# Optimization experiments

Hardware: AMD Instinct MI355X
Metric: run time of the kernel (lower is better)

The kernel has to match this reference:

```python
import jax, jax.numpy as jnp
import numpy as np

B, L, H, V = 16, 512, 256, 32000
HALF = H // 2
EPS_LN = 1e-5
EPS_NORM = 1e-12


def setup_inputs() -> dict:
    key = jax.random.key(0)
    ks = jax.random.split(key, 9)
    s = 0.02
    return {
        "seq": jax.random.randint(ks[0], (B, L), 0, V),
        "embed": jax.random.normal(ks[1], (V, H), jnp.float32) * s,
        "W1": jax.random.normal(ks[2], (2 * H, H), jnp.float32) * s,
        "b1": jnp.zeros((2 * H,), jnp.float32),
        "W2": jax.random.normal(ks[3], (H, 2 * H), jnp.float32) * s,
        "b2": jnp.zeros((H,), jnp.float32),
        "gamma": jnp.ones((H,), jnp.float32),
        "beta": jnp.zeros((H,), jnp.float32),
        "W_sem": jax.random.normal(ks[4], (HALF, H), jnp.float32) * s,
        "W_epi": jax.random.normal(ks[5], (HALF, H), jnp.float32) * s,
        "W_rp": jax.random.normal(ks[6], (H, H), jnp.float32) * s,
        "b_rp": jnp.zeros((H,), jnp.float32),
        "W_out": jax.random.normal(ks[7], (V, H), jnp.float32) * s,
        "b_out": jnp.zeros((V,), jnp.float32),
    }


def _l2norm(x):
    # F.normalize(dim=-1): x / max(||x||, eps)
    n = jnp.sqrt(jnp.sum(x * x, axis=-1, keepdims=True))
    return x / jnp.maximum(n, EPS_NORM)


def reference(seq, embed, W1, b1, W2, b2, gamma, beta, W_sem, W_epi, W_rp, b_rp, W_out, b_out):
    h = embed[seq]                                   # [B, L, H]
    ff = jnp.maximum(h @ W1.T + b1, 0.0) @ W2.T + b2  # MLP with 2H hidden
    x = h + ff
    mu = jnp.mean(x, axis=-1, keepdims=True)
    var = jnp.var(x, axis=-1, keepdims=True)
    h = (x - mu) / jnp.sqrt(var + EPS_LN) * gamma + beta  # LayerNorm

    ks_all = jnp.einsum('blh,kh->blk', h, W_sem)     # [B, L, HALF]
    ke_all = jnp.einsum('blh,kh->blk', h, W_epi)

    def step(carry, kv):
        M_s, M_e = carry
        k_s, k_e = kv                                 # [B, HALF] each
        kns = _l2norm(k_s)
        kne = _l2norm(k_e)
        vps = jnp.einsum('bij,bj->bi', M_s, kns)      # read from fast weights
        vpe = jnp.einsum('bij,bj->bi', M_e, kne)
        M_s = M_s + jnp.einsum('bi,bj->bij', k_s - vps, kns)  # delta-rule write
        M_e = M_e + jnp.einsum('bi,bj->bij', k_e - vpe, kne)
        return (M_s, M_e), None

    M0 = jnp.zeros((B, HALF, HALF), h.dtype)
    # scan over timesteps 0..L-2 (time-major)
    (M_s, M_e), _ = jax.lax.scan(
        step, (M0, M0),
        (jnp.swapaxes(ks_all[:, :-1], 0, 1), jnp.swapaxes(ke_all[:, :-1], 0, 1)))

    cs = jnp.einsum('bij,bj->bi', M_s, ks_all[:, -1])  # read with last-token query
    ce = jnp.einsum('bij,bj->bi', M_e, ke_all[:, -1])
    c = jnp.concatenate([cs, ce], axis=-1)             # [B, H]
    r = c @ W_rp.T + b_rp
    return r @ W_out.T + b_out                          # [B, V]
```

## Files before the change

kernel.cpp:

```cpp
#include <hip/hip_runtime.h>

#define B_ 16
#define L_ 512
#define H_ 256
#define V_ 32000
#define HALF_ 128

typedef __attribute__((ext_vector_type(8))) short short8;
typedef __attribute__((ext_vector_type(4))) float floatx4;

__device__ __forceinline__ unsigned short f2bf(float x) {
  unsigned int u = __float_as_uint(x);
  unsigned int r = (u + 0x7FFFu + ((u >> 16) & 1u)) >> 16;
  return (unsigned short)r;
}

__global__ void gather_kernel(const int* __restrict__ seq, const float* __restrict__ embed,
                              float* __restrict__ h, unsigned short* __restrict__ hbf) {
  int token = blockIdx.x;
  int lane = threadIdx.x;
  int row = seq[token];
  float4 v = ((const float4*)(embed + (size_t)row * H_))[lane];
  ((float4*)(h + (size_t)token * H_))[lane] = v;
  ushort4 b;
  b.x = f2bf(v.x); b.y = f2bf(v.y); b.z = f2bf(v.z); b.w = f2bf(v.w);
  *(ushort4*)(hbf + (size_t)token * H_ + lane * 4) = b;
}

__global__ void wconv_kernel(const float* __restrict__ W1, const float* __restrict__ W2,
                             const float* __restrict__ Ws, const float* __restrict__ We,
                             unsigned short* __restrict__ W1b, unsigned short* __restrict__ W2b,
                             unsigned short* __restrict__ Wcb) {
  int i = blockIdx.x * 256 + threadIdx.x;
  if (i < 131072) W1b[i] = f2bf(W1[i]);
  else if (i < 262144) W2b[i - 131072] = f2bf(W2[i - 131072]);
  else if (i < 294912) Wcb[i - 262144] = f2bf(Ws[i - 262144]);
  else Wcb[i - 262144] = f2bf(We[i - 294912]);
}

template <bool RELU, bool BIAS, bool RES, bool OUT_BF16>
__global__ __launch_bounds__(256) void gemm_mfma(const unsigned short* __restrict__ A,
                                                 const unsigned short* __restrict__ Bw,
                                                 const float* __restrict__ bias,
                                                 const float* __restrict__ Res,
                                                 float* __restrict__ Cf,
                                                 unsigned short* __restrict__ Cb,
                                                 int M, int N, int K) {
  __shared__ unsigned short As[128 * 40];
  __shared__ unsigned short Bs[128 * 40];
  int tid = threadIdx.x;
  int wave = tid >> 6, lane = tid & 63;
  int wm = (wave >> 1) * 64, wn = (wave & 1) * 64;
  int quad = lane >> 4, l15 = lane & 15;
  int bm = blockIdx.y * 128, bn = blockIdx.x * 128;
  int sr = tid >> 2, sq = tid & 3;

  floatx4 zero = {0.f, 0.f, 0.f, 0.f};
  floatx4 acc[4][4];
#pragma unroll
  for (int fi = 0; fi < 4; fi++)
#pragma unroll
    for (int fj = 0; fj < 4; fj++) acc[fi][fj] = zero;

  for (int k0 = 0; k0 < K; k0 += 32) {
    uint4 av0 = *(const uint4*)(A + (size_t)(bm + sr) * K + k0 + sq * 8);
    uint4 av1 = *(const uint4*)(A + (size_t)(bm + 64 + sr) * K + k0 + sq * 8);
    uint4 bv0 = *(const uint4*)(Bw + (size_t)(bn + sr) * K + k0 + sq * 8);
    uint4 bv1 = *(const uint4*)(Bw + (size_t)(bn + 64 + sr) * K + k0 + sq * 8);
    __syncthreads();
    *(uint4*)(As + sr * 40 + sq * 8) = av0;
    *(uint4*)(As + (64 + sr) * 40 + sq * 8) = av1;
    *(uint4*)(Bs + sr * 40 + sq * 8) = bv0;
    *(uint4*)(Bs + (64 + sr) * 40 + sq * 8) = bv1;
    __syncthreads();
    short8 af[4], bf[4];
#pragma unroll
    for (int f = 0; f < 4; f++) {
      af[f] = *(const short8*)(As + (wm + f * 16 + l15) * 40 + quad * 8);
      bf[f] = *(const short8*)(Bs + (wn + f * 16 + l15) * 40 + quad * 8);
    }
#pragma unroll
    for (int fi = 0; fi < 4; fi++)
#pragma unroll
      for (int fj = 0; fj < 4; fj++)
        acc[fi][fj] = __builtin_amdgcn_mfma_f32_16x16x32_bf16(af[fi], bf[fj], acc[fi][fj], 0, 0, 0);
  }

#pragma unroll
  for (int fi = 0; fi < 4; fi++) {
#pragma unroll
    for (int fj = 0; fj < 4; fj++) {
      int col = bn + wn + fj * 16 + l15;
      float bb = BIAS ? bias[col] : 0.f;
#pragma unroll
      for (int rg = 0; rg < 4; rg++) {
        int row = bm + wm + fi * 16 + quad * 4 + rg;
        float v = acc[fi][fj][rg] + bb;
        if (RES) v += Res[(size_t)row * N + col];
        if (RELU) v = fmaxf(v, 0.f);
        if (OUT_BF16) Cb[(size_t)row * N + col] = f2bf(v);
        else Cf[(size_t)row * N + col] = v;
      }
    }
  }
}

__global__ void ln_kernel(const float* __restrict__ x, const float* __restrict__ gamma,
                          const float* __restrict__ beta, unsigned short* __restrict__ yb) {
  int row = blockIdx.x;
  int lane = threadIdx.x;
  float4 v = ((const float4*)(x + (size_t)row * H_))[lane];
  float s = v.x + v.y + v.z + v.w;
  float sq = v.x * v.x + v.y * v.y + v.z * v.z + v.w * v.w;
#pragma unroll
  for (int off = 32; off >= 1; off >>= 1) {
    s += __shfl_xor(s, off);
    sq += __shfl_xor(sq, off);
  }
  float mu = s * (1.f / H_);
  float var = sq * (1.f / H_) - mu * mu;
  float inv = rsqrtf(var + 1e-5f);
  float4 g = ((const float4*)gamma)[lane];
  float4 b = ((const float4*)beta)[lane];
  ushort4 o;
  o.x = f2bf((v.x - mu) * inv * g.x + b.x);
  o.y = f2bf((v.y - mu) * inv * g.y + b.y);
  o.z = f2bf((v.z - mu) * inv * g.z + b.z);
  o.w = f2bf((v.w - mu) * inv * g.w + b.w);
  *(ushort4*)(yb + (size_t)row * H_ + lane * 4) = o;
}

__global__ __launch_bounds__(256) void normalize_kernel(const float* __restrict__ kcat,
                                                        unsigned short* __restrict__ khat) {
  int e = blockIdx.x * 4 + (threadIdx.x >> 6);
  int lane = threadIdx.x & 63;
  int idxm = e >> 9, t = e & 511;
  int b = idxm >> 1, mat = idxm & 1;
  const float* kp = kcat + ((size_t)b * L_ + t) * 256 + mat * 128;
  float2 v = ((const float2*)kp)[lane];
  float s = v.x * v.x + v.y * v.y;
#pragma unroll
  for (int off = 32; off >= 1; off >>= 1) s += __shfl_xor(s, off);
  float inv = 1.f / fmaxf(sqrtf(s), 1e-12f);
  ushort2 o;
  o.x = f2bf(v.x * inv);
  o.y = f2bf(v.y * inv);
  *(ushort2*)(khat + (size_t)e * HALF_ + lane * 2) = o;
}

template <int CTRL>
__device__ __forceinline__ float dpp_xor_add(float x) {
  int y = __builtin_amdgcn_mov_dpp(__float_as_int(x), CTRL, 0xf, 0xf, true);
  return x + __int_as_float(y);
}

#define BL_(u) __uint_as_float((u) << 16)
#define BH_(u) __uint_as_float((u) & 0xffff0000u)

#define SCAN_STEP(PK, PR)                                              \
  do {                                                                 \
    float k0 = BL_(PK.x), k1 = BH_(PK.x), k2 = BL_(PK.y), k3 = BH_(PK.y), \
          k4 = BL_(PK.z), k5 = BH_(PK.z), k6 = BL_(PK.w), k7 = BH_(PK.w); \
    float pa = m[0] * k0 + m[1] * k1, pb = m[2] * k2 + m[3] * k3,      \
          pc = m[4] * k4 + m[5] * k5, pd = m[6] * k6 + m[7] * k7;      \
    float p = (pa + pb) + (pc + pd);                                   \
    p = dpp_xor_add<0xB1>(p);                                          \
    p = dpp_xor_add<0x4E>(p);                                          \
    p = dpp_xor_add<0x141>(p);                                         \
    p = dpp_xor_add<0x140>(p);                                         \
    float sS = PR - p;                                                 \
    m[0] += sS * k0; m[1] += sS * k1; m[2] += sS * k2; m[3] += sS * k3; \
    m[4] += sS * k4; m[5] += sS * k5; m[6] += sS * k6; m[7] += sS * k7; \
  } while (0)

__global__ __launch_bounds__(256) void scan_kernel(const float* __restrict__ kcat,
                                                   const unsigned short* __restrict__ khat,
                                                   float* __restrict__ c) {
  int bid = blockIdx.x;
  int idxm = bid & 31;
  int rg = bid >> 5;
  int b = idxm >> 1, mat = idxm & 1;
  const unsigned short* kh = khat + (size_t)idxm * L_ * HALF_;
  const float* kbase = kcat + (size_t)b * L_ * 256 + mat * HALF_;

  int tid = threadIdx.x;
  int seg = tid & 15;
  int rl = tid >> 4;
  int r = rg * 16 + rl;
  int c0 = seg * 8;
  const float* krow = kbase + r;

  float m[8];
#pragma unroll
  for (int g = 0; g < 8; g++) m[g] = 0.f;

  uint4 pk[4];
  float pr[4];
#pragma unroll
  for (int u = 0; u < 4; u++) {
    pk[u] = *(const uint4*)(kh + (size_t)u * HALF_ + c0);
    pr[u] = krow[(size_t)u * 256];
  }

  for (int t = 0; t < 508; t += 4) {
#pragma unroll
    for (int u = 0; u < 4; u++) {
      int tt = t + u;
      uint4 nk = *(const uint4*)(kh + (size_t)(tt + 4) * HALF_ + c0);
      float nr = krow[(size_t)(tt + 4) * 256];
      SCAN_STEP(pk[u], pr[u]);
      pk[u] = nk;
      pr[u] = nr;
    }
  }
  SCAN_STEP(pk[0], pr[0]);
  SCAN_STEP(pk[1], pr[1]);
  SCAN_STEP(pk[2], pr[2]);

  float4 qa = *(const float4*)(kbase + (size_t)511 * 256 + c0);
  float4 qb = *(const float4*)(kbase + (size_t)511 * 256 + c0 + 4);
  float pa = m[0] * qa.x + m[1] * qa.y, pb2 = m[2] * qa.z + m[3] * qa.w;
  float pc = m[4] * qb.x + m[5] * qb.y, pd = m[6] * qb.z + m[7] * qb.w;
  float p = (pa + pb2) + (pc + pd);
  p = dpp_xor_add<0xB1>(p);
  p = dpp_xor_add<0x4E>(p);
  p = dpp_xor_add<0x141>(p);
  p = dpp_xor_add<0x140>(p);
  if (seg == 0) c[(size_t)b * H_ + mat * HALF_ + r] = p;
}

__global__ void rp_kernel(const float* __restrict__ c, const float* __restrict__ Wrp,
                          const float* __restrict__ brp, float* __restrict__ r) {
  int b = blockIdx.x;
  int n = threadIdx.x;
  __shared__ float cs[H_];
  cs[n] = c[(size_t)b * H_ + n];
  __syncthreads();
  const float4* w4 = (const float4*)(Wrp + (size_t)n * H_);
  const float4* c4 = (const float4*)cs;
  float acc = 0.f;
#pragma unroll 8
  for (int k = 0; k < H_ / 4; k++) {
    float4 w = w4[k], cc = c4[k];
    acc += w.x * cc.x + w.y * cc.y + w.z * cc.z + w.w * cc.w;
  }
  r[(size_t)b * H_ + n] = acc + brp[n];
}

__global__ __launch_bounds__(256) void out_kernel(const float* __restrict__ r,
                                                  const float* __restrict__ Wout,
                                                  const float* __restrict__ bout,
                                                  float* __restrict__ out) {
  __shared__ float rs[B_ * H_];
  int tid = threadIdx.x;
#pragma unroll
  for (int q = 0; q < (B_ * H_) / 256; q++) rs[q * 256 + tid] = r[q * 256 + tid];
  __syncthreads();
  int v = blockIdx.x * 256 + tid;
  const float4* w4 = (const float4*)(Wout + (size_t)v * H_);
  float acc[B_];
#pragma unroll
  for (int b = 0; b < B_; b++) acc[b] = 0.f;
  for (int k = 0; k < H_ / 4; k++) {
    float4 w = w4[k];
#pragma unroll
    for (int b = 0; b < B_; b++) {
      float4 rr = *(const float4*)&rs[b * H_ + 4 * k];
      acc[b] += w.x * rr.x + w.y * rr.y + w.z * rr.z + w.w * rr.w;
    }
  }
  float bo = bout[v];
#pragma unroll
  for (int b = 0; b < B_; b++) out[(size_t)b * V_ + v] = acc[b] + bo;
}

extern "C" void kernel_launch(void* const* d_in, const int* in_sizes, int n_in,
                              void* d_out, int out_size, void* d_ws, size_t ws_size,
                              hipStream_t stream) {
  const int* seq = (const int*)d_in[0];
  const float* embed = (const float*)d_in[1];
  const float* W1 = (const float*)d_in[2];
  const float* b1 = (const float*)d_in[3];
  const float* W2 = (const float*)d_in[4];
  const float* b2 = (const float*)d_in[5];
  const float* gamma = (const float*)d_in[6];
  const float* beta = (const float*)d_in[7];
  const float* Wsem = (const float*)d_in[8];
  const float* Wepi = (const float*)d_in[9];
  const float* Wrp = (const float*)d_in[10];
  const float* brp = (const float*)d_in[11];
  const float* Wout = (const float*)d_in[12];
  const float* bout = (const float*)d_in[13];
  float* out = (float*)d_out;

  float* ws = (float*)d_ws;
  float* h = ws;
  float* x = h;
  float* kcat = ws + 2097152;
  unsigned short* a1b = (unsigned short*)kcat;
  unsigned short* hbf = (unsigned short*)(ws + 4194304);
  unsigned short* hnb = (unsigned short*)(ws + 5242880);
  unsigned short* khat = (unsigned short*)(ws + 6291456);
  unsigned short* W1b = (unsigned short*)(ws + 7340032);
  unsigned short* W2b = (unsigned short*)(ws + 7405568);
  unsigned short* Wcb = (unsigned short*)(ws + 7471104);
  float* c = ws + 7503872;
  float* r = ws + 7508000;

  gather_kernel<<<8192, 64, 0, stream>>>(seq, embed, h, hbf);
  wconv_kernel<<<1280, 256, 0, stream>>>(W1, W2, Wsem, Wepi, W1b, W2b, Wcb);
  gemm_mfma<true, true, false, true><<<dim3(4, 64), 256, 0, stream>>>(
      hbf, W1b, b1, nullptr, nullptr, a1b, 8192, 512, 256);
  gemm_mfma<false, true, true, false><<<dim3(2, 64), 256, 0, stream>>>(
      a1b, W2b, b2, h, x, nullptr, 8192, 256, 512);
  ln_kernel<<<8192, 64, 0, stream>>>(x, gamma, beta, hnb);
  gemm_mfma<false, false, false, false><<<dim3(2, 64), 256, 0, stream>>>(
      hnb, Wcb, nullptr, nullptr, kcat, nullptr, 8192, 256, 256);
  normalize_kernel<<<4096, 256, 0, stream>>>(kcat, khat);
  scan_kernel<<<256, 256, 0, stream>>>(kcat, khat, c);
  rp_kernel<<<16, 256, 0, stream>>>(c, Wrp, brp, r);
  out_kernel<<<125, 256, 0, stream>>>(r, Wout, bout, out);
}
```

Before: 249.9 us.

## Fuse gather, layernorm and normalization into GEMMs; retile scan and output kernels

The embedding gather is folded into the first GEMM, which converts to bf16 on load. The residual add and LayerNorm move into the epilogue of a new second GEMM that computes full rows. The key projection now does the L2 normalization itself and writes fp32 normalized keys plus a transposed raw-key layout for the scan. The scan runs in fp32 with an 8-step prefetch window, and the output GEMV is split across 4 threads per vocab row with staged, coalesced stores. This removes several launches and intermediate round trips through memory, at the cost of larger fp32 key buffers and lower GEMM tile occupancy (32-row tiles).

```diff
diff --git a/kernel.cpp b/kernel.cpp
--- a/kernel.cpp
+++ b/kernel.cpp
@@ -15,22 +15,27 @@
   return (unsigned short)r;
 }
 
-__global__ void gather_kernel(const int* __restrict__ seq, const float* __restrict__ embed,
-                              float* __restrict__ h, unsigned short* __restrict__ hbf) {
-  int token = blockIdx.x;
-  int lane = threadIdx.x;
-  int row = seq[token];
-  float4 v = ((const float4*)(embed + (size_t)row * H_))[lane];
-  ((float4*)(h + (size_t)token * H_))[lane] = v;
-  ushort4 b;
-  b.x = f2bf(v.x); b.y = f2bf(v.y); b.z = f2bf(v.z); b.w = f2bf(v.w);
-  *(ushort4*)(hbf + (size_t)token * H_ + lane * 4) = b;
-}
-
-__global__ void wconv_kernel(const float* __restrict__ W1, const float* __restrict__ W2,
-                             const float* __restrict__ Ws, const float* __restrict__ We,
-                             unsigned short* __restrict__ W1b, unsigned short* __restrict__ W2b,
-                             unsigned short* __restrict__ Wcb) {
+template <int CTRL>
+__device__ __forceinline__ float dpp_xor_add(float x) {
+  int y = __builtin_amdgcn_mov_dpp(__float_as_int(x), CTRL, 0xf, 0xf, true);
+  return x + __int_as_float(y);
+}
+
+__device__ __forceinline__ float redu16(float p) {
+  p = dpp_xor_add<0xB1>(p);
+  p = dpp_xor_add<0x4E>(p);
+  p = dpp_xor_add<0x141>(p);
+  p = dpp_xor_add<0x140>(p);
+  return p;
+}
+
+__global__ __launch_bounds__(256) void wconv_kernel(const float* __restrict__ W1,
+                                                    const float* __restrict__ W2,
+                                                    const float* __restrict__ Ws,
+                                                    const float* __restrict__ We,
+                                                    unsigned short* __restrict__ W1b,
+                                                    unsigned short* __restrict__ W2b,
+                                                    unsigned short* __restrict__ Wcb) {
   int i = blockIdx.x * 256 + threadIdx.x;
   if (i < 131072) W1b[i] = f2bf(W1[i]);
   else if (i < 262144) W2b[i - 131072] = f2bf(W2[i - 131072]);
@@ -38,14 +43,22 @@
   else Wcb[i - 262144] = f2bf(We[i - 294912]);
 }
 
-template <bool RELU, bool BIAS, bool RES, bool OUT_BF16>
-__global__ __launch_bounds__(256) void gemm_mfma(const unsigned short* __restrict__ A,
-                                                 const unsigned short* __restrict__ Bw,
-                                                 const float* __restrict__ bias,
-                                                 const float* __restrict__ Res,
-                                                 float* __restrict__ Cf,
-                                                 unsigned short* __restrict__ Cb,
-                                                 int M, int N, int K) {
+__device__ __forceinline__ uint4 load8cvt(const float* p) {
+  float4 a = ((const float4*)p)[0];
+  float4 b = ((const float4*)p)[1];
+  uint4 r;
+  r.x = (unsigned)f2bf(a.x) | ((unsigned)f2bf(a.y) << 16);
+  r.y = (unsigned)f2bf(a.z) | ((unsigned)f2bf(a.w) << 16);
+  r.z = (unsigned)f2bf(b.x) | ((unsigned)f2bf(b.y) << 16);
+  r.w = (unsigned)f2bf(b.z) | ((unsigned)f2bf(b.w) << 16);
+  return r;
+}
+
+__global__ __launch_bounds__(256) void gemm1_kernel(const int* __restrict__ seq,
+                                                    const float* __restrict__ embed,
+                                                    const unsigned short* __restrict__ W1b,
+                                                    const float* __restrict__ b1,
+                                                    unsigned short* __restrict__ a1b) {
   __shared__ unsigned short As[128 * 40];
   __shared__ unsigned short Bs[128 * 40];
   int tid = threadIdx.x;
@@ -55,18 +68,26 @@
   int bm = blockIdx.y * 128, bn = blockIdx.x * 128;
   int sr = tid >> 2, sq = tid & 3;
 
+  int tok0 = seq[bm + sr];
+  int tok1 = seq[bm + 64 + sr];
+
   floatx4 zero = {0.f, 0.f, 0.f, 0.f};
-  floatx4 acc[4][4];
-#pragma unroll
-  for (int fi = 0; fi < 4; fi++)
+  floatx4 acc[2][4];
+#pragma unroll
+  for (int fi = 0; fi < 2; fi++)
 #pragma unroll
     for (int fj = 0; fj < 4; fj++) acc[fi][fj] = zero;
-
-  for (int k0 = 0; k0 < K; k0 += 32) {
-    uint4 av0 = *(const uint4*)(A + (size_t)(bm + sr) * K + k0 + sq * 8);
-    uint4 av1 = *(const uint4*)(A + (size_t)(bm + 64 + sr) * K + k0 + sq * 8);
-    uint4 bv0 = *(const uint4*)(Bw + (size_t)(bn + sr) * K + k0 + sq * 8);
-    uint4 bv1 = *(const uint4*)(Bw + (size_t)(bn + 64 + sr) * K + k0 + sq * 8);
+  floatx4 acc2[2][4];
+#pragma unroll
+  for (int fi = 0; fi < 2; fi++)
+#pragma unroll
+    for (int fj = 0; fj < 4; fj++) acc2[fi][fj] = zero;
+
+  for (int k0 = 0; k0 < 256; k0 += 32) {
+    uint4 av0 = load8cvt(embed + (size_t)tok0 * H_ + k0 + sq * 8);
+    uint4 av1 = load8cvt(embed + (size_t)tok1 * H_ + k0 + sq * 8);
+    uint4 bv0 = *(const uint4*)(W1b + (size_t)(bn + sr) * 256 + k0 + sq * 8);
+    uint4 bv1 = *(const uint4*)(W1b + (size_t)(bn + 64 + sr) * 256 + k0 + sq * 8);
     __syncthreads();
     *(uint4*)(As + sr * 40 + sq * 8) = av0;
     *(uint4*)(As + (64 + sr) * 40 + sq * 8) = av1;
@@ -80,10 +101,12 @@
       bf[f] = *(const short8*)(Bs + (wn + f * 16 + l15) * 40 + quad * 8);
     }
 #pragma unroll
-    for (int fi = 0; fi < 4; fi++)
-#pragma unroll
-      for (int fj = 0; fj < 4; fj++)
+    for (int fi = 0; fi < 2; fi++)
+#pragma unroll
+      for (int fj = 0; fj < 4; fj++) {
         acc[fi][fj] = __builtin_amdgcn_mfma_f32_16x16x32_bf16(af[fi], bf[fj], acc[fi][fj], 0, 0, 0);
+        acc2[fi][fj] = __builtin_amdgcn_mfma_f32_16x16x32_bf16(af[fi + 2], bf[fj], acc2[fi][fj], 0, 0, 0);
+      }
   }
 
 #pragma unroll
@@ -91,141 +114,274 @@
 #pragma unroll
     for (int fj = 0; fj < 4; fj++) {
       int col = bn + wn + fj * 16 + l15;
-      float bb = BIAS ? bias[col] : 0.f;
+      float bb = b1[col];
+      floatx4 a = (fi < 2) ? acc[fi][fj] : acc2[fi - 2][fj];
 #pragma unroll
       for (int rg = 0; rg < 4; rg++) {
         int row = bm + wm + fi * 16 + quad * 4 + rg;
-        float v = acc[fi][fj][rg] + bb;
-        if (RES) v += Res[(size_t)row * N + col];
-        if (RELU) v = fmaxf(v, 0.f);
-        if (OUT_BF16) Cb[(size_t)row * N + col] = f2bf(v);
-        else Cf[(size_t)row * N + col] = v;
+        float v = fmaxf(a[rg] + bb, 0.f);
+        a1b[(size_t)row * 512 + col] = f2bf(v);
       }
     }
   }
 }
 
-__global__ void ln_kernel(const float* __restrict__ x, const float* __restrict__ gamma,
-                          const float* __restrict__ beta, unsigned short* __restrict__ yb) {
-  int row = blockIdx.x;
-  int lane = threadIdx.x;
-  float4 v = ((const float4*)(x + (size_t)row * H_))[lane];
-  float s = v.x + v.y + v.z + v.w;
-  float sq = v.x * v.x + v.y * v.y + v.z * v.z + v.w * v.w;
-#pragma unroll
-  for (int off = 32; off >= 1; off >>= 1) {
-    s += __shfl_xor(s, off);
-    sq += __shfl_xor(sq, off);
-  }
-  float mu = s * (1.f / H_);
-  float var = sq * (1.f / H_) - mu * mu;
-  float inv = rsqrtf(var + 1e-5f);
-  float4 g = ((const float4*)gamma)[lane];
-  float4 b = ((const float4*)beta)[lane];
-  ushort4 o;
-  o.x = f2bf((v.x - mu) * inv * g.x + b.x);
-  o.y = f2bf((v.y - mu) * inv * g.y + b.y);
-  o.z = f2bf((v.z - mu) * inv * g.z + b.z);
-  o.w = f2bf((v.w - mu) * inv * g.w + b.w);
-  *(ushort4*)(yb + (size_t)row * H_ + lane * 4) = o;
-}
-
-__global__ __launch_bounds__(256) void normalize_kernel(const float* __restrict__ kcat,
-                                                        unsigned short* __restrict__ khat) {
-  int e = blockIdx.x * 4 + (threadIdx.x >> 6);
-  int lane = threadIdx.x & 63;
-  int idxm = e >> 9, t = e & 511;
-  int b = idxm >> 1, mat = idxm & 1;
-  const float* kp = kcat + ((size_t)b * L_ + t) * 256 + mat * 128;
-  float2 v = ((const float2*)kp)[lane];
-  float s = v.x * v.x + v.y * v.y;
-#pragma unroll
-  for (int off = 32; off >= 1; off >>= 1) s += __shfl_xor(s, off);
-  float inv = 1.f / fmaxf(sqrtf(s), 1e-12f);
-  ushort2 o;
-  o.x = f2bf(v.x * inv);
-  o.y = f2bf(v.y * inv);
-  *(ushort2*)(khat + (size_t)e * HALF_ + lane * 2) = o;
-}
-
-template <int CTRL>
-__device__ __forceinline__ float dpp_xor_add(float x) {
-  int y = __builtin_amdgcn_mov_dpp(__float_as_int(x), CTRL, 0xf, 0xf, true);
-  return x + __int_as_float(y);
-}
-
-#define BL_(u) __uint_as_float((u) << 16)
-#define BH_(u) __uint_as_float((u) & 0xffff0000u)
-
-#define SCAN_STEP(PK, PR)                                              \
-  do {                                                                 \
-    float k0 = BL_(PK.x), k1 = BH_(PK.x), k2 = BL_(PK.y), k3 = BH_(PK.y), \
-          k4 = BL_(PK.z), k5 = BH_(PK.z), k6 = BL_(PK.w), k7 = BH_(PK.w); \
-    float pa = m[0] * k0 + m[1] * k1, pb = m[2] * k2 + m[3] * k3,      \
-          pc = m[4] * k4 + m[5] * k5, pd = m[6] * k6 + m[7] * k7;      \
-    float p = (pa + pb) + (pc + pd);                                   \
-    p = dpp_xor_add<0xB1>(p);                                          \
-    p = dpp_xor_add<0x4E>(p);                                          \
-    p = dpp_xor_add<0x141>(p);                                         \
-    p = dpp_xor_add<0x140>(p);                                         \
-    float sS = PR - p;                                                 \
-    m[0] += sS * k0; m[1] += sS * k1; m[2] += sS * k2; m[3] += sS * k3; \
-    m[4] += sS * k4; m[5] += sS * k5; m[6] += sS * k6; m[7] += sS * k7; \
+__global__ __launch_bounds__(256) void mlp2_kernel(const unsigned short* __restrict__ a1b,
+                                                   const unsigned short* __restrict__ W2b,
+                                                   const float* __restrict__ b2,
+                                                   const int* __restrict__ seq,
+                                                   const float* __restrict__ embed,
+                                                   const float* __restrict__ gamma,
+                                                   const float* __restrict__ beta,
+                                                   unsigned short* __restrict__ hnb) {
+  __shared__ unsigned short As[32 * 40];
+  __shared__ unsigned short Bs[256 * 40];
+  __shared__ float stats[2][2][32];
+  int tid = threadIdx.x;
+  int wave = tid >> 6, lane = tid & 63;
+  int wm = (wave >> 1) * 16, wnh = wave & 1, wn = wnh * 128;
+  int quad = lane >> 4, l15 = lane & 15;
+  int bm = blockIdx.x * 32;
+
+  floatx4 zero = {0.f, 0.f, 0.f, 0.f};
+  floatx4 acc[8];
+#pragma unroll
+  for (int fj = 0; fj < 8; fj++) acc[fj] = zero;
+
+  for (int k0 = 0; k0 < 512; k0 += 32) {
+    uint4 av;
+    if (tid < 128) {
+      int sr = tid >> 2, sq = tid & 3;
+      av = *(const uint4*)(a1b + (size_t)(bm + sr) * 512 + k0 + sq * 8);
+    }
+    uint4 bv[4];
+#pragma unroll
+    for (int q = 0; q < 4; q++) {
+      int unit = q * 256 + tid;
+      int row = unit >> 2, sq2 = unit & 3;
+      bv[q] = *(const uint4*)(W2b + (size_t)row * 512 + k0 + sq2 * 8);
+    }
+    __syncthreads();
+    if (tid < 128) {
+      int sr = tid >> 2, sq = tid & 3;
+      *(uint4*)(As + sr * 40 + sq * 8) = av;
+    }
+#pragma unroll
+    for (int q = 0; q < 4; q++) {
+      int unit = q * 256 + tid;
+      int row = unit >> 2, sq2 = unit & 3;
+      *(uint4*)(Bs + row * 40 + sq2 * 8) = bv[q];
+    }
+    __syncthreads();
+    short8 af = *(const short8*)(As + (wm + l15) * 40 + quad * 8);
+    short8 bf[8];
+#pragma unroll
+    for (int fj = 0; fj < 8; fj++)
+      bf[fj] = *(const short8*)(Bs + (wn + fj * 16 + l15) * 40 + quad * 8);
+#pragma unroll
+    for (int fj = 0; fj < 8; fj++)
+      acc[fj] = __builtin_amdgcn_mfma_f32_16x16x32_bf16(af, bf[fj], acc[fj], 0, 0, 0);
+  }
+
+  int seqv[4];
+#pragma unroll
+  for (int rg = 0; rg < 4; rg++) seqv[rg] = seq[bm + wm + quad * 4 + rg];
+  float v[8][4];
+#pragma unroll
+  for (int fj = 0; fj < 8; fj++) {
+    int col = wn + fj * 16 + l15;
+    float bb = b2[col];
+#pragma unroll
+    for (int rg = 0; rg < 4; rg++)
+      v[fj][rg] = acc[fj][rg] + bb + embed[(size_t)seqv[rg] * H_ + col];
+  }
+  float s_[4], q_[4];
+#pragma unroll
+  for (int rg = 0; rg < 4; rg++) {
+    float s = 0.f, q = 0.f;
+#pragma unroll
+    for (int fj = 0; fj < 8; fj++) {
+      s += v[fj][rg];
+      q += v[fj][rg] * v[fj][rg];
+    }
+    s_[rg] = redu16(s);
+    q_[rg] = redu16(q);
+  }
+  if (l15 == 0) {
+#pragma unroll
+    for (int rg = 0; rg < 4; rg++) {
+      int rlocal = wm + quad * 4 + rg;
+      stats[wnh][0][rlocal] = s_[rg];
+      stats[wnh][1][rlocal] = q_[rg];
+    }
+  }
+  __syncthreads();
+  float mu[4], inv[4];
+#pragma unroll
+  for (int rg = 0; rg < 4; rg++) {
+    int rlocal = wm + quad * 4 + rg;
+    float sum = stats[0][0][rlocal] + stats[1][0][rlocal];
+    float ssq = stats[0][1][rlocal] + stats[1][1][rlocal];
+    mu[rg] = sum * (1.f / H_);
+    float var = ssq * (1.f / H_) - mu[rg] * mu[rg];
+    inv[rg] = rsqrtf(var + 1e-5f);
+  }
+#pragma unroll
+  for (int fj = 0; fj < 8; fj++) {
+    int col = wn + fj * 16 + l15;
+    float g = gamma[col], be = beta[col];
+#pragma unroll
+    for (int rg = 0; rg < 4; rg++) {
+      int row = bm + wm + quad * 4 + rg;
+      float y = (v[fj][rg] - mu[rg]) * inv[rg] * g + be;
+      hnb[(size_t)row * H_ + col] = f2bf(y);
+    }
+  }
+}
+
+__global__ __launch_bounds__(256) void kproj_kernel(const unsigned short* __restrict__ hnb,
+                                                    const unsigned short* __restrict__ Wcb,
+                                                    float* __restrict__ khat,
+                                                    float* __restrict__ kT) {
+  __shared__ unsigned short As[32 * 40];
+  __shared__ unsigned short Bs[256 * 40];
+  int tid = threadIdx.x;
+  int wave = tid >> 6, lane = tid & 63;
+  int wm = (wave >> 1) * 16, wnh = wave & 1, wn = wnh * 128;
+  int quad = lane >> 4, l15 = lane & 15;
+  int bm = blockIdx.x * 32;
+
+  floatx4 zero = {0.f, 0.f, 0.f, 0.f};
+  floatx4 acc[8];
+#pragma unroll
+  for (int fj = 0; fj < 8; fj++) acc[fj] = zero;
+
+  for (int k0 = 0; k0 < 256; k0 += 32) {
+    uint4 av;
+    if (tid < 128) {
+      int sr = tid >> 2, sq = tid & 3;
+      av = *(const uint4*)(hnb + (size_t)(bm + sr) * H_ + k0 + sq * 8);
+    }
+    uint4 bv[4];
+#pragma unroll
+    for (int q = 0; q < 4; q++) {
+      int unit = q * 256 + tid;
+      int row = unit >> 2, sq2 = unit & 3;
+      bv[q] = *(const uint4*)(Wcb + (size_t)row * H_ + k0 + sq2 * 8);
+    }
+    __syncthreads();
+    if (tid < 128) {
+      int sr = tid >> 2, sq = tid & 3;
+      *(uint4*)(As + sr * 40 + sq * 8) = av;
+    }
+#pragma unroll
+    for (int q = 0; q < 4; q++) {
+      int unit = q * 256 + tid;
+      int row = unit >> 2, sq2 = unit & 3;
+      *(uint4*)(Bs + row * 40 + sq2 * 8) = bv[q];
+    }
+    __syncthreads();
+    short8 af = *(const short8*)(As + (wm + l15) * 40 + quad * 8);
+    short8 bf[8];
+#pragma unroll
+    for (int fj = 0; fj < 8; fj++)
+      bf[fj] = *(const short8*)(Bs + (wn + fj * 16 + l15) * 40 + quad * 8);
+#pragma unroll
+    for (int fj = 0; fj < 8; fj++)
+      acc[fj] = __builtin_amdgcn_mfma_f32_16x16x32_bf16(af, bf[fj], acc[fj], 0, 0, 0);
+  }
+
+  int b = bm >> 9;
+  int idxm = b * 2 + wnh;
+  int tloc0 = (bm & 511) + wm + quad * 4;
+  float inv[4];
+#pragma unroll
+  for (int rg = 0; rg < 4; rg++) {
+    float ssq = 0.f;
+#pragma unroll
+    for (int fj = 0; fj < 8; fj++) ssq += acc[fj][rg] * acc[fj][rg];
+    ssq = redu16(ssq);
+    inv[rg] = 1.f / fmaxf(sqrtf(ssq), 1e-12f);
+  }
+#pragma unroll
+  for (int fj = 0; fj < 8; fj++) {
+    int ch = fj * 16 + l15;
+#pragma unroll
+    for (int rg = 0; rg < 4; rg++)
+      khat[((size_t)idxm * L_ + tloc0 + rg) * HALF_ + ch] = acc[fj][rg] * inv[rg];
+    float4 raw = {acc[fj][0], acc[fj][1], acc[fj][2], acc[fj][3]};
+    *(float4*)(kT + (size_t)idxm * (HALF_ * L_) + (size_t)ch * L_ + tloc0) = raw;
+  }
+}
+
+#define STEP8(KP, PR)                                                      \
+  do {                                                                     \
+    float t0_ = m[0] * KP[0] + m[1] * KP[1];                               \
+    float t1_ = m[2] * KP[2] + m[3] * KP[3];                               \
+    float t2_ = m[4] * KP[4] + m[5] * KP[5];                               \
+    float t3_ = m[6] * KP[6] + m[7] * KP[7];                               \
+    float p_ = (t0_ + t1_) + (t2_ + t3_);                                  \
+    p_ = redu16(p_);                                                       \
+    float s_ = PR - p_;                                                    \
+    m[0] += s_ * KP[0]; m[1] += s_ * KP[1]; m[2] += s_ * KP[2];            \
+    m[3] += s_ * KP[3]; m[4] += s_ * KP[4]; m[5] += s_ * KP[5];            \
+    m[6] += s_ * KP[6]; m[7] += s_ * KP[7];                                \
   } while (0)
 
-__global__ __launch_bounds__(256) void scan_kernel(const float* __restrict__ kcat,
-                                                   const unsigned short* __restrict__ khat,
-                                                   float* __restrict__ c) {
+__global__ __launch_bounds__(256, 1) void scan_kernel(const float* __restrict__ khat,
+                                                      const float* __restrict__ kT,
+                                                      float* __restrict__ c) {
   int bid = blockIdx.x;
   int idxm = bid & 31;
   int rg = bid >> 5;
   int b = idxm >> 1, mat = idxm & 1;
-  const unsigned short* kh = khat + (size_t)idxm * L_ * HALF_;
-  const float* kbase = kcat + (size_t)b * L_ * 256 + mat * HALF_;
+  const float* kh = khat + (size_t)idxm * L_ * HALF_;
+  const float* kTi = kT + (size_t)idxm * HALF_ * L_;
 
   int tid = threadIdx.x;
   int seg = tid & 15;
   int rl = tid >> 4;
   int r = rg * 16 + rl;
   int c0 = seg * 8;
-  const float* krow = kbase + r;
+  const float* krow = kTi + (size_t)r * L_;
 
   float m[8];
 #pragma unroll
   for (int g = 0; g < 8; g++) m[g] = 0.f;
 
-  uint4 pk[4];
-  float pr[4];
-#pragma unroll
-  for (int u = 0; u < 4; u++) {
-    pk[u] = *(const uint4*)(kh + (size_t)u * HALF_ + c0);
-    pr[u] = krow[(size_t)u * 256];
-  }
-
-  for (int t = 0; t < 508; t += 4) {
-#pragma unroll
-    for (int u = 0; u < 4; u++) {
-      int tt = t + u;
-      uint4 nk = *(const uint4*)(kh + (size_t)(tt + 4) * HALF_ + c0);
-      float nr = krow[(size_t)(tt + 4) * 256];
-      SCAN_STEP(pk[u], pr[u]);
-      pk[u] = nk;
-      pr[u] = nr;
-    }
-  }
-  SCAN_STEP(pk[0], pr[0]);
-  SCAN_STEP(pk[1], pr[1]);
-  SCAN_STEP(pk[2], pr[2]);
-
-  float4 qa = *(const float4*)(kbase + (size_t)511 * 256 + c0);
-  float4 qb = *(const float4*)(kbase + (size_t)511 * 256 + c0 + 4);
-  float pa = m[0] * qa.x + m[1] * qa.y, pb2 = m[2] * qa.z + m[3] * qa.w;
-  float pc = m[4] * qb.x + m[5] * qb.y, pd = m[6] * qb.z + m[7] * qb.w;
-  float p = (pa + pb2) + (pc + pd);
-  p = dpp_xor_add<0xB1>(p);
-  p = dpp_xor_add<0x4E>(p);
-  p = dpp_xor_add<0x141>(p);
-  p = dpp_xor_add<0x140>(p);
+  float pk[8][8];
+  float kr[8];
+#pragma unroll
+  for (int u = 0; u < 8; u++) {
+    *(float4*)&pk[u][0] = *(const float4*)(kh + (size_t)u * HALF_ + c0);
+    *(float4*)&pk[u][4] = *(const float4*)(kh + (size_t)u * HALF_ + c0 + 4);
+  }
+  *(float4*)&kr[0] = *(const float4*)(krow);
+  *(float4*)&kr[4] = *(const float4*)(krow + 4);
+
+  for (int i = 0; i < 63; i++) {
+    int nt = (i + 1) * 8;
+    const float* knext = kh + (size_t)nt * HALF_ + c0;
+#pragma unroll
+    for (int u = 0; u < 8; u++) {
+      STEP8(pk[u], kr[u]);
+      *(float4*)&pk[u][0] = *(const float4*)(knext + (size_t)u * HALF_);
+      *(float4*)&pk[u][4] = *(const float4*)(knext + (size_t)u * HALF_ + 4);
+      if (u == 3) *(float4*)&kr[0] = *(const float4*)(krow + nt);
+      if (u == 7) *(float4*)&kr[4] = *(const float4*)(krow + nt + 4);
+    }
+  }
+#pragma unroll
+  for (int u = 0; u < 7; u++) STEP8(pk[u], kr[u]);
+
+  float q[8];
+#pragma unroll
+  for (int j = 0; j < 8; j++) q[j] = kTi[(size_t)(c0 + j) * L_ + 511];
+  float t0 = m[0] * q[0] + m[1] * q[1];
+  float t1 = m[2] * q[2] + m[3] * q[3];
+  float t2 = m[4] * q[4] + m[5] * q[5];
+  float t3 = m[6] * q[6] + m[7] * q[7];
+  float p = redu16((t0 + t1) + (t2 + t3));
   if (seg == 0) c[(size_t)b * H_ + mat * HALF_ + r] = p;
 }
 
@@ -251,27 +407,49 @@
                                                   const float* __restrict__ Wout,
                                                   const float* __restrict__ bout,
                                                   float* __restrict__ out) {
-  __shared__ float rs[B_ * H_];
+  __shared__ float rs[16 * 272];
+  __shared__ float obuf[16 * 68];
   int tid = threadIdx.x;
 #pragma unroll
-  for (int q = 0; q < (B_ * H_) / 256; q++) rs[q * 256 + tid] = r[q * 256 + tid];
+  for (int q = 0; q < 16; q++) {
+    int idx = q * 256 + tid;
+    int bb = idx >> 8, cc = idx & 255;
+    rs[bb * 272 + cc + 4 * (cc >> 6)] = r[idx];
+  }
   __syncthreads();
-  int v = blockIdx.x * 256 + tid;
-  const float4* w4 = (const float4*)(Wout + (size_t)v * H_);
-  float acc[B_];
-#pragma unroll
-  for (int b = 0; b < B_; b++) acc[b] = 0.f;
-  for (int k = 0; k < H_ / 4; k++) {
-    float4 w = w4[k];
-#pragma unroll
-    for (int b = 0; b < B_; b++) {
-      float4 rr = *(const float4*)&rs[b * H_ + 4 * k];
-      acc[b] += w.x * rr.x + w.y * rr.y + w.z * rr.z + w.w * rr.w;
+  int row = tid >> 2, part = tid & 3;
+  int v = blockIdx.x * 64 + row;
+  const float4* w4 = (const float4*)(Wout + (size_t)v * H_ + part * 64);
+  float acc[16];
+#pragma unroll
+  for (int bb = 0; bb < 16; bb++) acc[bb] = 0.f;
+#pragma unroll 4
+  for (int j = 0; j < 16; j++) {
+    float4 w = w4[j];
+#pragma unroll
+    for (int bb = 0; bb < 16; bb++) {
+      float4 rv = *(const float4*)&rs[bb * 272 + part * 68 + j * 4];
+      acc[bb] += w.x * rv.x + w.y * rv.y + w.z * rv.z + w.w * rv.w;
     }
   }
   float bo = bout[v];
 #pragma unroll
-  for (int b = 0; b < B_; b++) out[(size_t)b * V_ + v] = acc[b] + bo;
+  for (int bb = 0; bb < 16; bb++) {
+    acc[bb] = dpp_xor_add<0xB1>(acc[bb]);
+    acc[bb] = dpp_xor_add<0x4E>(acc[bb]);
+  }
+#pragma unroll
+  for (int q = 0; q < 4; q++) {
+    int bb = part * 4 + q;
+    obuf[bb * 68 + row] = acc[bb] + bo;
+  }
+  __syncthreads();
+#pragma unroll
+  for (int q = 0; q < 4; q++) {
+    int idx = q * 256 + tid;
+    int bb = idx >> 6, vl = idx & 63;
+    out[(size_t)bb * V_ + blockIdx.x * 64 + vl] = obuf[bb * 68 + vl];
+  }
 }
 
 extern "C" void kernel_launch(void* const* d_in, const int* in_sizes, int n_in,
@@ -294,30 +472,21 @@
   float* out = (float*)d_out;
 
   float* ws = (float*)d_ws;
-  float* h = ws;
-  float* x = h;
-  float* kcat = ws + 2097152;
-  unsigned short* a1b = (unsigned short*)kcat;
-  unsigned short* hbf = (unsigned short*)(ws + 4194304);
-  unsigned short* hnb = (unsigned short*)(ws + 5242880);
-  unsigned short* khat = (unsigned short*)(ws + 6291456);
+  unsigned short* a1b = (unsigned short*)ws;
+  unsigned short* hnb = (unsigned short*)(ws + 2097152);
+  float* khat = ws + 3145728;
+  float* kT = ws + 5242880;
   unsigned short* W1b = (unsigned short*)(ws + 7340032);
   unsigned short* W2b = (unsigned short*)(ws + 7405568);
   unsigned short* Wcb = (unsigned short*)(ws + 7471104);
   float* c = ws + 7503872;
-  float* r = ws + 7508000;
-
-  gather_kernel<<<8192, 64, 0, stream>>>(seq, embed, h, hbf);
+  float* r = ws + 7507968;
+
   wconv_kernel<<<1280, 256, 0, stream>>>(W1, W2, Wsem, Wepi, W1b, W2b, Wcb);
-  gemm_mfma<true, true, false, true><<<dim3(4, 64), 256, 0, stream>>>(
-      hbf, W1b, b1, nullptr, nullptr, a1b, 8192, 512, 256);
-  gemm_mfma<false, true, true, false><<<dim3(2, 64), 256, 0, stream>>>(
-      a1b, W2b, b2, h, x, nullptr, 8192, 256, 512);
-  ln_kernel<<<8192, 64, 0, stream>>>(x, gamma, beta, hnb);
-  gemm_mfma<false, false, false, false><<<dim3(2, 64), 256, 0, stream>>>(
-      hnb, Wcb, nullptr, nullptr, kcat, nullptr, 8192, 256, 256);
-  normalize_kernel<<<4096, 256, 0, stream>>>(kcat, khat);
-  scan_kernel<<<256, 256, 0, stream>>>(kcat, khat, c);
+  gemm1_kernel<<<dim3(4, 64), 256, 0, stream>>>(seq, embed, W1b, b1, a1b);
+  mlp2_kernel<<<256, 256, 0, stream>>>(a1b, W2b, b2, seq, embed, gamma, beta, hnb);
+  kproj_kernel<<<256, 256, 0, stream>>>(hnb, Wcb, khat, kT);
+  scan_kernel<<<256, 256, 0, stream>>>(khat, kT, c);
   rp_kernel<<<16, 256, 0, stream>>>(c, Wrp, brp, r);
-  out_kernel<<<125, 256, 0, stream>>>(r, Wout, bout, out);
-}
+  out_kernel<<<500, 256, 0, stream>>>(r, Wout, bout, out);
+}
```

New measurement: 246.9 us. About the same (-1.2%).
